# Performance work log

Measured on AMD Instinct MI355X. Metric: run time of the kernel, lower is better.

Reference implementation:

```python
import jax, jax.numpy as jnp
import numpy as np

B, S, H, L, V = 32, 128, 1024, 2, 32000


def setup_inputs() -> dict:
    key = jax.random.key(0)
    ks = jax.random.split(key, 9)
    scale = 1.0 / np.sqrt(H)
    return {
        "x": jax.random.randint(ks[0], (B, 1), 0, V),
        "hidden": jax.random.normal(ks[1], (L, B, H), jnp.float32) * 0.1,
        "cell": jax.random.normal(ks[2], (L, B, H), jnp.float32) * 0.1,
        "target": jax.random.randint(ks[3], (B, S), 0, V),
        "tf_ratio": 1,  # teacher forcing always on -> deterministic
        "emb": jax.random.normal(ks[4], (V, H), jnp.float32) * 0.02,
        "w_ih": jax.random.normal(ks[5], (L, 4 * H, H), jnp.float32) * scale,
        "w_hh": jax.random.normal(ks[6], (L, 4 * H, H), jnp.float32) * scale,
        "b_ih": jax.random.normal(ks[7], (L, 4 * H), jnp.float32) * scale,
        "b_hh": jax.random.normal(ks[8], (L, 4 * H), jnp.float32) * scale,
    }


def _lstm_decode(tokens, h0, c0, emb, w_ih, w_hh, b_ih, b_hh):
    # tokens: [B,S] int; embed all teacher-forced inputs at once
    x_seq = emb[tokens]                      # [B,S,H]
    x_tbh = jnp.swapaxes(x_seq, 0, 1)        # [S,B,H]
    n_layers = h0.shape[0]

    def step(carry, x_t):
        h, c = carry                         # each [L,B,H]
        inp = x_t                            # [B,H]
        hs, cs = [], []
        for l in range(n_layers):
            # PyTorch gate order: i, f, g, o
            z = inp @ w_ih[l].T + h[l] @ w_hh[l].T + b_ih[l] + b_hh[l]
            i, f, g, o = jnp.split(z, 4, axis=-1)
            c_new = jax.nn.sigmoid(f) * c[l] + jax.nn.sigmoid(i) * jnp.tanh(g)
            h_new = jax.nn.sigmoid(o) * jnp.tanh(c_new)
            hs.append(h_new)
            cs.append(c_new)
            inp = h_new
        return (jnp.stack(hs), jnp.stack(cs)), inp

    _, outs = jax.lax.scan(step, (h0, c0), x_tbh)  # outs: [S,B,H]
    out = jnp.swapaxes(outs, 0, 1)                 # [B,S,H]
    # tied-weight projection to vocab
    return jnp.einsum("bsh,vh->bsv", out, emb)     # [B,S,V]


def reference(x, hidden, cell, target, tf_ratio, emb, w_ih, w_hh, b_ih, b_hh):
    # tf_ratio == 1: step 0 consumes x, step i>=1 consumes target[:, i]
    tokens = jnp.concatenate([x, target[:, 1:]], axis=1)  # [B,S]
    return _lstm_decode(tokens, hidden, cell, emb, w_ih, w_hh, b_ih, b_hh)
```

## Files before the change

kernel.cpp:

```cpp
#include <hip/hip_runtime.h>
#include <stdint.h>


typedef __attribute__((ext_vector_type(8))) short short8;
typedef __attribute__((ext_vector_type(4))) float f32x4;

#define MFMA16(a, b, c) __builtin_amdgcn_mfma_f32_16x16x32_bf16((a), (b), (c), 0, 0, 0)

__device__ __forceinline__ unsigned short f2bf(float f) {
  union { float f; unsigned int u; } v; v.f = f;
  unsigned int u = v.u;
  return (unsigned short)((u + 0x7fffu + ((u >> 16) & 1u)) >> 16);
}

__device__ __forceinline__ void gload_lds16(const unsigned short* g, unsigned short* l) {
  __builtin_amdgcn_global_load_lds(
      (const __attribute__((address_space(1))) void*)g,
      (__attribute__((address_space(3))) void*)l, 16, 0, 0);
}

__device__ __forceinline__ void st_u32_dev(unsigned* p, unsigned v) {
  __hip_atomic_store(p, v, __ATOMIC_RELAXED, __HIP_MEMORY_SCOPE_AGENT);
}
__device__ __forceinline__ unsigned ld_u32_dev(const unsigned* p) {
  return __hip_atomic_load(p, __ATOMIC_RELAXED, __HIP_MEMORY_SCOPE_AGENT);
}


__global__ void cvt_bf16_k(const float* __restrict__ s, unsigned short* __restrict__ d, int n4) {
  int i = blockIdx.x * blockDim.x + threadIdx.x;
  int st = gridDim.x * blockDim.x;
  for (; i < n4; i += st) {
    float4 v = ((const float4*)s)[i];
    ushort4 o;
    o.x = f2bf(v.x); o.y = f2bf(v.y); o.z = f2bf(v.z); o.w = f2bf(v.w);
    ((ushort4*)d)[i] = o;
  }
}

__global__ void bias_sum_k(const float* __restrict__ a, const float* __restrict__ b,
                           float* __restrict__ o, int n) {
  int i = blockIdx.x * blockDim.x + threadIdx.x;
  if (i < n) o[i] = a[i] + b[i];
}

__global__ void embed_k(const int* __restrict__ x, const int* __restrict__ tgt,
                        const float* __restrict__ emb, unsigned short* __restrict__ xseq) {
  int row = blockIdx.x;
  int t = row >> 5, b = row & 31;
  int tok = (t == 0) ? x[b] : tgt[b * 128 + t];
  const float4* e = (const float4*)(emb + (size_t)tok * 1024);
  ushort4* o = (ushort4*)(xseq + (size_t)row * 1024);
  int i = threadIdx.x;
  float4 v = e[i];
  ushort4 u;
  u.x = f2bf(v.x); u.y = f2bf(v.y); u.z = f2bf(v.z); u.w = f2bf(v.w);
  o[i] = u;
}


__global__ __launch_bounds__(256, 2) void gemm_bf16_k(
    const unsigned short* __restrict__ A, const unsigned short* __restrict__ B,
    float* __restrict__ C, const float* __restrict__ bias, int N, int permC) {
  __shared__ __align__(16) unsigned short smem[32768];
  const int tid = threadIdx.x;
  const int lane = tid & 63;
  const int w = tid >> 6;
  const int wm = w >> 1, wn = w & 1;
  const int xcd = blockIdx.x & 7;
  const int idx = blockIdx.x >> 3;
  const int nBase = (idx >> 2) * 128;
  const int mBase = (xcd * 4 + (idx & 3)) * 128;
  const int lr = lane & 15, lk = lane >> 4;
  const int K = 1024;

  const int srow = tid >> 3;
  const int scol = (tid & 7) ^ (srow & 7);
  const int wchunk = tid & 192;

  f32x4 acc[4][4];
#pragma unroll
  for (int i = 0; i < 4; ++i)
#pragma unroll
    for (int j = 0; j < 4; ++j) acc[i][j] = (f32x4){0.f, 0.f, 0.f, 0.f};

  const unsigned short* Ag = A + (size_t)mBase * K;
  const unsigned short* Bg = B + (size_t)nBase * K;

  auto stage = [&](int buf, int kt) {
    unsigned short* Ab = smem + buf * 16384;
    unsigned short* Bb = Ab + 8192;
#pragma unroll
    for (int r = 0; r < 4; ++r) {
      int row = r * 32 + srow;
      gload_lds16(Ag + (size_t)row * K + kt * 64 + scol * 8, &Ab[(r * 256 + wchunk) * 8]);
      gload_lds16(Bg + (size_t)row * K + kt * 64 + scol * 8, &Bb[(r * 256 + wchunk) * 8]);
    }
  };

  stage(0, 0);
  __syncthreads();
  for (int kt = 0; kt < 16; ++kt) {
    int cur = kt & 1;
    if (kt < 15) stage(cur ^ 1, kt + 1);
    const unsigned short* Ac = smem + cur * 16384;
    const unsigned short* Bc = Ac + 8192;
#pragma unroll
    for (int ks = 0; ks < 2; ++ks) {
      short8 a[4], b[4];
#pragma unroll
      for (int mf = 0; mf < 4; ++mf) {
        int row = wm * 64 + mf * 16 + lr;
        int cc = (ks * 4 + lk) ^ (row & 7);
        a[mf] = *(const short8*)&Ac[row * 64 + cc * 8];
      }
#pragma unroll
      for (int nf = 0; nf < 4; ++nf) {
        int row = wn * 64 + nf * 16 + lr;
        int cc = (ks * 4 + lk) ^ (row & 7);
        b[nf] = *(const short8*)&Bc[row * 64 + cc * 8];
      }
#pragma unroll
      for (int mf = 0; mf < 4; ++mf)
#pragma unroll
        for (int nf = 0; nf < 4; ++nf)
          acc[mf][nf] = MFMA16(a[mf], b[nf], acc[mf][nf]);
    }
    __syncthreads();
  }

  float* cst = (float*)smem;
#pragma unroll
  for (int r = 0; r < 4; ++r) {
    __syncthreads();
#pragma unroll
    for (int nf = 0; nf < 4; ++nf) {
      int col = wn * 64 + nf * 16 + lr;
      float bv = bias ? bias[nBase + col] : 0.f;
#pragma unroll
      for (int i = 0; i < 4; ++i)
        cst[(wm * 16 + lk * 4 + i) * 132 + col] = acc[r][nf][i] + bv;
    }
    __syncthreads();
#pragma unroll
    for (int pss = 0; pss < 4; ++pss) {
      int idxq = pss * 256 + tid;
      int rl = idxq >> 5, cq = idxq & 31;
      int ar = mBase + (rl >> 4) * 64 + r * 16 + (rl & 15);
      int cr = permC ? ((ar & 31) * 128 + (ar >> 5)) : ar;
      f32x4 v = *(const f32x4*)&cst[rl * 132 + cq * 4];
      __builtin_nontemporal_store(v, (f32x4*)&C[(size_t)cr * N + nBase + cq * 4]);
    }
  }
}


struct PParams {
  const float* zx0;
  const unsigned short* whh0;
  const unsigned short* wih1;
  const unsigned short* whh1;
  const float* bsum1;
  const float* cell;
  unsigned short* h0hist;
  const unsigned short* h1init;
  unsigned short* outb;
  unsigned int* slots0;
  unsigned int* slots1;
  unsigned int* queue;
  const unsigned short* embB;
  float* outC;
  int njobs;
};

__device__ __forceinline__ void proj_tile(int j, bool valid, int ltid, char* smbase,
                                          const unsigned short* Aout,
                                          const unsigned short* Bemb, float* C) {
  const int mB = j / 250, nB = j % 250;
  const int mBase = mB * 128, nBase = nB * 128;
  const int lane = ltid & 63;
  const int w4 = ltid >> 6;
  const int wm = w4 >> 1, wn = w4 & 1;
  const int lr = lane & 15, lk = lane >> 4;
  const int srow = ltid >> 3;
  const int scol = (ltid & 7) ^ (srow & 7);
  const int wchunk = ltid & 192;
  unsigned short* smem = (unsigned short*)smbase;

  f32x4 acc[4][4];
#pragma unroll
  for (int i = 0; i < 4; ++i)
#pragma unroll
    for (int q = 0; q < 4; ++q) acc[i][q] = (f32x4){0.f, 0.f, 0.f, 0.f};

  const unsigned short* Ag = Aout + (size_t)mBase * 1024;
  const unsigned short* Bg = Bemb + (size_t)nBase * 1024;

  auto stage = [&](int buf, int kt) {
    if (!valid) return;
    unsigned short* Ab = smem + buf * 16384;
    unsigned short* Bb = Ab + 8192;
#pragma unroll
    for (int r = 0; r < 4; ++r) {
      int row = r * 32 + srow;
      gload_lds16(Ag + (size_t)row * 1024 + kt * 64 + scol * 8, &Ab[(r * 256 + wchunk) * 8]);
      gload_lds16(Bg + (size_t)row * 1024 + kt * 64 + scol * 8, &Bb[(r * 256 + wchunk) * 8]);
    }
  };

  stage(0, 0);
  __syncthreads();
  for (int kt = 0; kt < 16; ++kt) {
    int cur = kt & 1;
    if (kt < 15) stage(cur ^ 1, kt + 1);
    const unsigned short* Ac = smem + cur * 16384;
    const unsigned short* Bc = Ac + 8192;
    if (valid) {
#pragma unroll
      for (int ks = 0; ks < 2; ++ks) {
        short8 a[4], b[4];
#pragma unroll
        for (int mf = 0; mf < 4; ++mf) {
          int row = wm * 64 + mf * 16 + lr;
          int cc = (ks * 4 + lk) ^ (row & 7);
          a[mf] = *(const short8*)&Ac[row * 64 + cc * 8];
        }
#pragma unroll
        for (int nf = 0; nf < 4; ++nf) {
          int row = wn * 64 + nf * 16 + lr;
          int cc = (ks * 4 + lk) ^ (row & 7);
          b[nf] = *(const short8*)&Bc[row * 64 + cc * 8];
        }
#pragma unroll
        for (int mf = 0; mf < 4; ++mf)
#pragma unroll
          for (int nf = 0; nf < 4; ++nf)
            acc[mf][nf] = MFMA16(a[mf], b[nf], acc[mf][nf]);
      }
    }
    __syncthreads();
  }

  float* cst = (float*)smem;
#pragma unroll
  for (int r = 0; r < 4; ++r) {
    __syncthreads();
    if (valid) {
#pragma unroll
      for (int nf = 0; nf < 4; ++nf) {
        int col = wn * 64 + nf * 16 + lr;
#pragma unroll
        for (int i = 0; i < 4; ++i)
          cst[(wm * 16 + lk * 4 + i) * 132 + col] = acc[r][nf][i];
      }
    }
    __syncthreads();
    if (valid) {
#pragma unroll
      for (int pss = 0; pss < 4; ++pss) {
        int idxq = pss * 256 + ltid;
        int rl = idxq >> 5, cq = idxq & 31;
        int ar = mBase + (rl >> 4) * 64 + r * 16 + (rl & 15);
        int cr = (ar & 31) * 128 + (ar >> 5);
        f32x4 v = *(const f32x4*)&cst[rl * 132 + cq * 4];
        __builtin_nontemporal_store(v, (f32x4*)&C[(size_t)cr * 32000 + nBase + cq * 4]);
      }
    }
  }
}

__global__ __launch_bounds__(512, 1) void lstm_persist_k(PParams P) {
  const int tid = threadIdx.x;
  const int lane = tid & 63;
  const int w = tid >> 6;
  const int lr = lane & 15, lkk = lane >> 4;

  __shared__ __align__(16) char pool[149504];
  __shared__ int jbase;
  unsigned short* wlds = (unsigned short*)pool;
  float* zraw = (float*)(pool + 131072);

  if (blockIdx.x < 64) {
    const int u0 = blockIdx.x * 16;
    const int m = w >> 2;
    const int gp = (w >> 1) & 1;
    const int kh = w & 1;
    const int g0 = gp * 2, g1 = gp * 2 + 1;

    for (int f = w; f < 128; f += 8) {
      int gg = f >> 5, kc = f & 31;
      const unsigned short* src =
          P.whh0 + (size_t)(gg * 1024 + u0 + lr) * 1024 + kc * 32 + lkk * 8;
      *(short8*)&wlds[f * 512 + lane * 8] = *(const short8*)src;
    }
    const int fb = tid >> 3;
    const int jp = tid & 7;
    float creg[2] = {0.f, 0.f};
    if (tid < 256) {
      creg[0] = P.cell[fb * 1024 + u0 + 2 * jp];
      creg[1] = P.cell[fb * 1024 + u0 + 2 * jp + 1];
    }
    __syncthreads();

    for (int i = 0; i < 128; ++i) {
      if (i > 0 && tid < 64) {
        const unsigned tgt = (unsigned)i;
        while (true) {
          unsigned v = ld_u32_dev(&P.slots0[tid * 32]);
          if (__all(v >= tgt)) break;
          __builtin_amdgcn_s_sleep(1);
        }
      }
      __syncthreads();

      float2 zr[4];
      if (tid < 256) {
        const float2* br = (const float2*)(P.zx0 + (size_t)i * 131072 + fb * 4096 + u0 + 2 * jp);
#pragma unroll
        for (int q = 0; q < 4; ++q) zr[q] = br[q * 512];
      }
      f32x4 acc0 = {0.f, 0.f, 0.f, 0.f}, acc1 = {0.f, 0.f, 0.f, 0.f};
      const unsigned short* ap =
          P.h0hist + (size_t)i * 32768 + (size_t)(m * 16 + lr) * 1024 + kh * 512 + lkk * 8;
#pragma unroll
      for (int g4 = 0; g4 < 2; ++g4) {
        short8 a[8];
#pragma unroll
        for (int q = 0; q < 8; ++q) a[q] = *(const short8*)(ap + (g4 * 8 + q) * 32);
#pragma unroll
        for (int q = 0; q < 8; ++q) {
          int kc = kh * 16 + g4 * 8 + q;
          short8 b0 = *(const short8*)&wlds[(g0 * 32 + kc) * 512 + lane * 8];
          short8 b1 = *(const short8*)&wlds[(g1 * 32 + kc) * 512 + lane * 8];
          acc0 = MFMA16(a[q], b0, acc0);
          acc1 = MFMA16(a[q], b1, acc1);
        }
      }
#pragma unroll
      for (int j = 0; j < 4; ++j) {
        zraw[(kh * 32 + m * 16 + lkk * 4 + j) * 72 + g0 * 16 + lr] = acc0[j];
        zraw[(kh * 32 + m * 16 + lkk * 4 + j) * 72 + g1 * 16 + lr] = acc1[j];
      }
      __syncthreads();

      if (tid < 256) {
        unsigned hv = 0;
#pragma unroll
        for (int u = 0; u < 2; ++u) {
          int j = 2 * jp + u;
          float zi = zraw[fb * 72 + j]      + zraw[(32 + fb) * 72 + j]      + ((u == 0) ? zr[0].x : zr[0].y);
          float zf = zraw[fb * 72 + 16 + j] + zraw[(32 + fb) * 72 + 16 + j] + ((u == 0) ? zr[1].x : zr[1].y);
          float zg = zraw[fb * 72 + 32 + j] + zraw[(32 + fb) * 72 + 32 + j] + ((u == 0) ? zr[2].x : zr[2].y);
          float zo = zraw[fb * 72 + 48 + j] + zraw[(32 + fb) * 72 + 48 + j] + ((u == 0) ? zr[3].x : zr[3].y);
          float ii = 1.f / (1.f + __expf(-zi));
          float ff = 1.f / (1.f + __expf(-zf));
          float gg = tanhf(zg);
          float oo = 1.f / (1.f + __expf(-zo));
          float cn = ff * creg[u] + ii * gg;
          creg[u] = cn;
          float hn = oo * tanhf(cn);
          hv |= ((unsigned)f2bf(hn)) << (16 * u);
        }
        st_u32_dev((unsigned*)&P.h0hist[(size_t)(i + 1) * 32768 + fb * 1024 + u0 + 2 * jp], hv);
      }
      __syncthreads();
      if (tid == 0) st_u32_dev(&P.slots0[blockIdx.x * 32], (unsigned)(i + 1));
    }
  } else if (blockIdx.x < 192) {
    const int u0 = (blockIdx.x - 64) * 8;
    const int slot = blockIdx.x - 64;
    const int mat = w >> 2;
    const int m = (w >> 1) & 1;
    const int kh = w & 1;

    for (int f = w; f < 128; f += 8) {
      int matf = f >> 6, nt = (f >> 5) & 1, kc = f & 31;
      int rr = nt * 16 + lr;
      int gate = rr >> 3, unit = rr & 7;
      const unsigned short* Wm = matf ? P.whh1 : P.wih1;
      const unsigned short* src =
          Wm + (size_t)(gate * 1024 + u0 + unit) * 1024 + kc * 32 + lkk * 8;
      *(short8*)&wlds[f * 512 + lane * 8] = *(const short8*)src;
    }
    const int fb = tid >> 2;
    const int jp = tid & 3;
    float creg[2] = {0.f, 0.f};
    float brg[4][2];
    if (tid < 128) {
      creg[0] = P.cell[32768 + fb * 1024 + u0 + 2 * jp];
      creg[1] = P.cell[32768 + fb * 1024 + u0 + 2 * jp + 1];
#pragma unroll
      for (int q = 0; q < 4; ++q) {
        brg[q][0] = P.bsum1[q * 1024 + u0 + 2 * jp];
        brg[q][1] = P.bsum1[q * 1024 + u0 + 2 * jp + 1];
      }
    }
    __syncthreads();

    for (int i = 1; i <= 128; ++i) {
      if (tid < 64) {
        const unsigned t0 = (unsigned)i, t1 = (unsigned)(i - 1);
        while (true) {
          bool ok = ld_u32_dev(&P.slots0[tid * 32]) >= t0;
          if (i > 1) {
            ok = ok && ld_u32_dev(&P.slots1[tid * 32]) >= t1
                    && ld_u32_dev(&P.slots1[(tid + 64) * 32]) >= t1;
          }
          if (__all(ok)) break;
          __builtin_amdgcn_s_sleep(2);
        }
      }
      __syncthreads();

      f32x4 acc0 = {0.f, 0.f, 0.f, 0.f}, acc1 = {0.f, 0.f, 0.f, 0.f};
      const unsigned short* ap;
      if (mat == 0) {
        ap = P.h0hist + (size_t)i * 32768 + (size_t)(m * 16 + lr) * 1024 + kh * 512 + lkk * 8;
      } else {
        const unsigned short* h1b =
            (i == 1) ? P.h1init : (P.outb + (size_t)(i - 2) * 32768);
        ap = h1b + (size_t)(m * 16 + lr) * 1024 + kh * 512 + lkk * 8;
      }
#pragma unroll
      for (int g4 = 0; g4 < 2; ++g4) {
        short8 a[8];
#pragma unroll
        for (int q = 0; q < 8; ++q) a[q] = *(const short8*)(ap + (g4 * 8 + q) * 32);
#pragma unroll
        for (int q = 0; q < 8; ++q) {
          int kc = kh * 16 + g4 * 8 + q;
          short8 b0 = *(const short8*)&wlds[(mat * 64 + 0 * 32 + kc) * 512 + lane * 8];
          short8 b1 = *(const short8*)&wlds[(mat * 64 + 1 * 32 + kc) * 512 + lane * 8];
          acc0 = MFMA16(a[q], b0, acc0);
          acc1 = MFMA16(a[q], b1, acc1);
        }
      }
      float* zp = zraw + (mat * 2 + kh) * 1152;
#pragma unroll
      for (int j = 0; j < 4; ++j) {
        zp[(m * 16 + lkk * 4 + j) * 36 + lr] = acc0[j];
        zp[(m * 16 + lkk * 4 + j) * 36 + 16 + lr] = acc1[j];
      }
      __syncthreads();

      if (tid < 128) {
        unsigned hv = 0;
#pragma unroll
        for (int u = 0; u < 2; ++u) {
          int j = 2 * jp + u;
          float z4[4];
#pragma unroll
          for (int q = 0; q < 4; ++q) {
            z4[q] = zraw[fb * 36 + q * 8 + j] + zraw[1152 + fb * 36 + q * 8 + j]
                  + zraw[2304 + fb * 36 + q * 8 + j] + zraw[3456 + fb * 36 + q * 8 + j]
                  + brg[q][u];
          }
          float ii = 1.f / (1.f + __expf(-z4[0]));
          float ff = 1.f / (1.f + __expf(-z4[1]));
          float gg = tanhf(z4[2]);
          float oo = 1.f / (1.f + __expf(-z4[3]));
          float cn = ff * creg[u] + ii * gg;
          creg[u] = cn;
          float hn = oo * tanhf(cn);
          hv |= ((unsigned)f2bf(hn)) << (16 * u);
        }
        st_u32_dev((unsigned*)&P.outb[(size_t)(i - 1) * 32768 + fb * 1024 + u0 + 2 * jp], hv);
      }
      __syncthreads();
      if (tid == 0) st_u32_dev(&P.slots1[slot * 32], (unsigned)i);
    }
  }

  while (true) {
    __syncthreads();
    if (tid == 0)
      jbase = (int)__hip_atomic_fetch_add(P.queue, 2u, __ATOMIC_RELAXED,
                                          __HIP_MEMORY_SCOPE_AGENT);
    __syncthreads();
    int base = jbase;
    if (base >= P.njobs) break;
    int j = base + (tid >> 8);
    bool valid = (j < P.njobs);
    int jmax = (base + 1 < P.njobs) ? base + 1 : base;
    int gateMB = jmax / 250;
    if (tid < 64) {
      unsigned tgt = (unsigned)(4 * gateMB + 4);
      if (tgt > 128u) tgt = 128u;
      while (true) {
        bool ok = ld_u32_dev(&P.slots1[tid * 32]) >= tgt &&
                  ld_u32_dev(&P.slots1[(tid + 64) * 32]) >= tgt;
        if (__all(ok)) break;
        __builtin_amdgcn_s_sleep(2);
      }
    }
    __syncthreads();
    proj_tile(j, valid, tid & 255, pool + (tid >> 8) * 65536, P.outb, P.embB, P.outC);
  }
}


extern "C" void kernel_launch(void* const* d_in, const int* in_sizes, int n_in,
                              void* d_out, int out_size, void* d_ws, size_t ws_size,
                              hipStream_t stream) {
  const int*   x      = (const int*)d_in[0];
  const float* hidden = (const float*)d_in[1];
  const float* cell   = (const float*)d_in[2];
  const int*   target = (const int*)d_in[3];
  const float* emb    = (const float*)d_in[5];
  const float* w_ih   = (const float*)d_in[6];
  const float* w_hh   = (const float*)d_in[7];
  const float* b_ih   = (const float*)d_in[8];
  const float* b_hh   = (const float*)d_in[9];
  float* out = (float*)d_out;
  char* ws = (char*)d_ws;

  unsigned short* emb_bf  = (unsigned short*)(ws);
  unsigned short* wih0_bf = (unsigned short*)(ws + 65536000);
  unsigned short* whh_bf  = (unsigned short*)(ws + 73924608);
  unsigned short* wih1_bf = (unsigned short*)(ws + 90701824);
  float*          bsum    = (float*)(ws + 99090432);
  unsigned short* outb    = (unsigned short*)(ws + 99123200);
  unsigned int*   barmem  = (unsigned int*)(ws + 107511808);
  unsigned short* h1init  = (unsigned short*)(ws + 107544576);

  const size_t WS_NEED = 107610112ull + 67108864ull + 8454144ull;
  const bool rich = (ws_size >= WS_NEED);
  float*          zx0    = rich ? (float*)(ws + 107610112)
                                : (float*)d_out;
  unsigned short* xseq   = rich ? (unsigned short*)d_out
                                : (unsigned short*)((char*)d_out + 67108864);
  unsigned short* h0hist = rich ? (unsigned short*)(ws + 174718976)
                                : (unsigned short*)((char*)d_out + 75497472);

  hipMemsetAsync(barmem, 0, 32768, stream);
  cvt_bf16_k<<<2048, 256, 0, stream>>>(emb, emb_bf, 8192000);
  cvt_bf16_k<<<1024, 256, 0, stream>>>(w_ih, wih0_bf, 1048576);
  cvt_bf16_k<<<2048, 256, 0, stream>>>(w_hh, whh_bf, 2097152);
  cvt_bf16_k<<<1024, 256, 0, stream>>>(w_ih + 4194304, wih1_bf, 1048576);
  cvt_bf16_k<<<32, 256, 0, stream>>>(hidden, h0hist, 8192);
  cvt_bf16_k<<<32, 256, 0, stream>>>(hidden + 32768, h1init, 8192);
  bias_sum_k<<<32, 256, 0, stream>>>(b_ih, b_hh, bsum, 8192);
  embed_k<<<4096, 256, 0, stream>>>(x, target, emb, xseq);

  gemm_bf16_k<<<1024, 256, 0, stream>>>(xseq, wih0_bf, zx0, bsum, 4096, 0);

  PParams pp;
  pp.zx0 = zx0;
  pp.whh0 = whh_bf;
  pp.wih1 = wih1_bf;
  pp.whh1 = whh_bf + 4194304;
  pp.bsum1 = bsum + 4096;
  pp.cell = cell;
  pp.h0hist = h0hist;
  pp.h1init = h1init;
  pp.outb = outb;
  pp.slots0 = barmem;
  pp.slots1 = barmem + 2048;
  pp.queue = barmem + 6144;
  pp.embB = emb_bf;
  pp.outC = out;
  pp.njobs = rich ? 8000 : 0;
  lstm_persist_k<<<rich ? 256 : 192, 512, 0, stream>>>(pp);

  if (!rich) {
    gemm_bf16_k<<<8000, 256, 0, stream>>>(outb, emb_bf, out, nullptr, 32000, 1);
  }
}
```

Before: 1.084 ms.

## Replace per-block barrier signalling with per-wave flags and merge setup launches

After: 1.173 ms. +8.2%, slower.

```diff
diff --git a/kernel.cpp b/kernel.cpp
--- a/kernel.cpp
+++ b/kernel.cpp
@@ -38,10 +38,24 @@
   }
 }
 
-__global__ void bias_sum_k(const float* __restrict__ a, const float* __restrict__ b,
-                           float* __restrict__ o, int n) {
-  int i = blockIdx.x * blockDim.x + threadIdx.x;
-  if (i < n) o[i] = a[i] + b[i];
+__global__ void init_small_k(const float* __restrict__ hidden,
+                             const float* __restrict__ b_ih, const float* __restrict__ b_hh,
+                             unsigned short* __restrict__ h0, unsigned short* __restrict__ h1,
+                             float* __restrict__ bsum) {
+  int bb = blockIdx.x;
+  int tid = threadIdx.x;
+  if (bb < 64) {
+    const float* src = hidden + (bb < 32 ? 0 : 32768);
+    unsigned short* dst = (bb < 32) ? h0 : h1;
+    int i = (bb & 31) * 256 + tid;
+    float4 v = ((const float4*)src)[i];
+    ushort4 u;
+    u.x = f2bf(v.x); u.y = f2bf(v.y); u.z = f2bf(v.z); u.w = f2bf(v.w);
+    ((ushort4*)dst)[i] = u;
+  } else {
+    int i = (bb - 64) * 256 + tid;
+    bsum[i] = b_ih[i] + b_hh[i];
+  }
 }
 
 __global__ void embed_k(const int* __restrict__ x, const int* __restrict__ tgt,
@@ -173,6 +187,19 @@
   int njobs;
 };
 
+__device__ __forceinline__ bool l0_ready(const unsigned* slots0, int lane, unsigned tgt) {
+  const unsigned* blk = slots0 + lane * 32;
+  bool ok = ld_u32_dev(blk + 0) >= tgt && ld_u32_dev(blk + 1) >= tgt &&
+            ld_u32_dev(blk + 2) >= tgt && ld_u32_dev(blk + 3) >= tgt;
+  return ok;
+}
+__device__ __forceinline__ bool l1_ready(const unsigned* slots1, int lane, unsigned tgt) {
+  const unsigned* a = slots1 + lane * 32;
+  const unsigned* b = slots1 + (lane + 64) * 32;
+  return ld_u32_dev(a) >= tgt && ld_u32_dev(a + 1) >= tgt &&
+         ld_u32_dev(b) >= tgt && ld_u32_dev(b + 1) >= tgt;
+}
+
 __device__ __forceinline__ void proj_tile(int j, bool valid, int ltid, char* smbase,
                                           const unsigned short* Aout,
                                           const unsigned short* Bemb, float* C) {
@@ -303,22 +330,18 @@
     __syncthreads();
 
     for (int i = 0; i < 128; ++i) {
-      if (i > 0 && tid < 64) {
-        const unsigned tgt = (unsigned)i;
-        while (true) {
-          unsigned v = ld_u32_dev(&P.slots0[tid * 32]);
-          if (__all(v >= tgt)) break;
-          __builtin_amdgcn_s_sleep(1);
-        }
-      }
-      __syncthreads();
-
       float2 zr[4];
       if (tid < 256) {
         const float2* br = (const float2*)(P.zx0 + (size_t)i * 131072 + fb * 4096 + u0 + 2 * jp);
 #pragma unroll
         for (int q = 0; q < 4; ++q) zr[q] = br[q * 512];
       }
+      if (i > 0 && tid < 64) {
+        const unsigned tgt = (unsigned)i;
+        while (!l0_ready(P.slots0, tid, tgt)) __builtin_amdgcn_s_sleep(1);
+      }
+      __syncthreads();
+
       f32x4 acc0 = {0.f, 0.f, 0.f, 0.f}, acc1 = {0.f, 0.f, 0.f, 0.f};
       const unsigned short* ap =
           P.h0hist + (size_t)i * 32768 + (size_t)(m * 16 + lr) * 1024 + kh * 512 + lkk * 8;
@@ -362,9 +385,9 @@
           hv |= ((unsigned)f2bf(hn)) << (16 * u);
         }
         st_u32_dev((unsigned*)&P.h0hist[(size_t)(i + 1) * 32768 + fb * 1024 + u0 + 2 * jp], hv);
-      }
-      __syncthreads();
-      if (tid == 0) st_u32_dev(&P.slots0[blockIdx.x * 32], (unsigned)(i + 1));
+        asm volatile("s_waitcnt vmcnt(0)" ::: "memory");
+        if (lane == 0) st_u32_dev(&P.slots0[blockIdx.x * 32 + w], (unsigned)(i + 1));
+      }
     }
   } else if (blockIdx.x < 192) {
     const int u0 = (blockIdx.x - 64) * 8;
@@ -401,11 +424,8 @@
       if (tid < 64) {
         const unsigned t0 = (unsigned)i, t1 = (unsigned)(i - 1);
         while (true) {
-          bool ok = ld_u32_dev(&P.slots0[tid * 32]) >= t0;
-          if (i > 1) {
-            ok = ok && ld_u32_dev(&P.slots1[tid * 32]) >= t1
-                    && ld_u32_dev(&P.slots1[(tid + 64) * 32]) >= t1;
-          }
+          bool ok = l0_ready(P.slots0, tid, t0);
+          if (i > 1) ok = ok && l1_ready(P.slots1, tid, t1);
           if (__all(ok)) break;
           __builtin_amdgcn_s_sleep(2);
         }
@@ -465,9 +485,9 @@
           hv |= ((unsigned)f2bf(hn)) << (16 * u);
         }
         st_u32_dev((unsigned*)&P.outb[(size_t)(i - 1) * 32768 + fb * 1024 + u0 + 2 * jp], hv);
-      }
-      __syncthreads();
-      if (tid == 0) st_u32_dev(&P.slots1[slot * 32], (unsigned)i);
+        asm volatile("s_waitcnt vmcnt(0)" ::: "memory");
+        if (lane == 0) st_u32_dev(&P.slots1[slot * 32 + w], (unsigned)i);
+      }
     }
   }
 
@@ -486,12 +506,7 @@
     if (tid < 64) {
       unsigned tgt = (unsigned)(4 * gateMB + 4);
       if (tgt > 128u) tgt = 128u;
-      while (true) {
-        bool ok = ld_u32_dev(&P.slots1[tid * 32]) >= tgt &&
-                  ld_u32_dev(&P.slots1[(tid + 64) * 32]) >= tgt;
-        if (__all(ok)) break;
-        __builtin_amdgcn_s_sleep(2);
-      }
+      while (!l1_ready(P.slots1, tid, tgt)) __builtin_amdgcn_s_sleep(2);
     }
     __syncthreads();
     proj_tile(j, valid, tid & 255, pool + (tid >> 8) * 65536, P.outb, P.embB, P.outC);
@@ -515,9 +530,8 @@
   char* ws = (char*)d_ws;
 
   unsigned short* emb_bf  = (unsigned short*)(ws);
-  unsigned short* wih0_bf = (unsigned short*)(ws + 65536000);
-  unsigned short* whh_bf  = (unsigned short*)(ws + 73924608);
-  unsigned short* wih1_bf = (unsigned short*)(ws + 90701824);
+  unsigned short* wih_bf  = (unsigned short*)(ws + 65536000);
+  unsigned short* whh_bf  = (unsigned short*)(ws + 82313216);
   float*          bsum    = (float*)(ws + 99090432);
   unsigned short* outb    = (unsigned short*)(ws + 99123200);
   unsigned int*   barmem  = (unsigned int*)(ws + 107511808);
@@ -534,20 +548,17 @@
 
   hipMemsetAsync(barmem, 0, 32768, stream);
   cvt_bf16_k<<<2048, 256, 0, stream>>>(emb, emb_bf, 8192000);
-  cvt_bf16_k<<<1024, 256, 0, stream>>>(w_ih, wih0_bf, 1048576);
+  cvt_bf16_k<<<2048, 256, 0, stream>>>(w_ih, wih_bf, 2097152);
   cvt_bf16_k<<<2048, 256, 0, stream>>>(w_hh, whh_bf, 2097152);
-  cvt_bf16_k<<<1024, 256, 0, stream>>>(w_ih + 4194304, wih1_bf, 1048576);
-  cvt_bf16_k<<<32, 256, 0, stream>>>(hidden, h0hist, 8192);
-  cvt_bf16_k<<<32, 256, 0, stream>>>(hidden + 32768, h1init, 8192);
-  bias_sum_k<<<32, 256, 0, stream>>>(b_ih, b_hh, bsum, 8192);
+  init_small_k<<<96, 256, 0, stream>>>(hidden, b_ih, b_hh, h0hist, h1init, bsum);
   embed_k<<<4096, 256, 0, stream>>>(x, target, emb, xseq);
 
-  gemm_bf16_k<<<1024, 256, 0, stream>>>(xseq, wih0_bf, zx0, bsum, 4096, 0);
+  gemm_bf16_k<<<1024, 256, 0, stream>>>(xseq, wih_bf, zx0, bsum, 4096, 0);
 
   PParams pp;
   pp.zx0 = zx0;
   pp.whh0 = whh_bf;
-  pp.wih1 = wih1_bf;
+  pp.wih1 = wih_bf + 4194304;
   pp.whh1 = whh_bf + 4194304;
   pp.bsum1 = bsum + 4096;
   pp.cell = cell;
```
